# Kernel optimization log

Measured on AMD Instinct MI355X. Metric: run time of the kernel, lower is better.

The kernel has to match this reference:

```python
import jax, jax.numpy as jnp
import numpy as np
import math

D_K = 1024
HEADS = 16
HEAD_DIM = 64

def setup_inputs() -> dict:
    key = jax.random.key(0)
    ks = jax.random.split(key, 9)
    B, S, E = 2, 2048, D_K
    sc = 0.02
    return {
        "x": jax.random.normal(ks[0], (B, S, E), dtype=jnp.float32),
        "mask": 1,
        "Wq": jax.random.normal(ks[1], (E, E), dtype=jnp.float32) * sc,
        "bq": jnp.zeros((E,), dtype=jnp.float32),
        "Wk": jax.random.normal(ks[2], (E, E), dtype=jnp.float32) * sc,
        "bk": jnp.zeros((E,), dtype=jnp.float32),
        "Wv": jax.random.normal(ks[3], (E, E), dtype=jnp.float32) * sc,
        "bv": jnp.zeros((E,), dtype=jnp.float32),
        "Wo": jax.random.normal(ks[4], (E, E), dtype=jnp.float32) * sc,
        "bo": jnp.zeros((E,), dtype=jnp.float32),
    }

def reference(x, mask, Wq, bq, Wk, bk, Wv, bv, Wo, bo):
    B, S, E = x.shape
    H, Dh = HEADS, HEAD_DIM
    # QKV projections; split heads: [B, H, S, Dh]
    q = (x @ Wq + bq).reshape(B, S, H, Dh).transpose(0, 2, 1, 3)
    k = (x @ Wk + bk).reshape(B, S, H, Dh).transpose(0, 2, 1, 3)
    v = (x @ Wv + bv).reshape(B, S, H, Dh).transpose(0, 2, 1, 3)
    # NOTE: original scales by sqrt(d_k) (full model dim), not sqrt(head_dim)
    scores = jnp.einsum('bhsd,bhtd->bhst', q, k) / math.sqrt(E)
    if mask:
        causal = jnp.tril(jnp.ones((S, S), dtype=bool))
        scores = jnp.where(causal[None, None], scores, jnp.float32(-1e9))
    attn = jax.nn.softmax(scores, axis=-1)
    out = jnp.einsum('bhst,bhtd->bhsd', attn, v)  # [B,H,S,Dh]
    out = out.transpose(0, 2, 1, 3).reshape(B, S, E)
    return out @ Wo + bo
```

## Files before the change

### kernel.cpp

```cpp
#include <hip/hip_runtime.h>

#define HEADS  16
#define DH     64
#define SEQ    2048
#define NBATCH 2
#define EMB    1024
#define MTOT   (NBATCH * SEQ)

#define QSCALE 0.045084220027780106f

typedef short  s16x8 __attribute__((ext_vector_type(8)));
typedef float  f32x4 __attribute__((ext_vector_type(4)));
typedef unsigned short u16;
typedef unsigned short u16x4 __attribute__((ext_vector_type(4)));

__device__ __forceinline__ u16 f2bf(float f) {
  unsigned u = __builtin_bit_cast(unsigned, f);
  u += 0x7fffu + ((u >> 16) & 1u);
  return (u16)(u >> 16);
}

__device__ __forceinline__ void gll16(const u16* g, u16* l) {
  __builtin_amdgcn_global_load_lds(
      (const __attribute__((address_space(1))) unsigned int*)g,
      (__attribute__((address_space(3))) unsigned int*)l, 16, 0, 0);
}

__global__ void cvt_x_kernel(const float* __restrict__ x, u16* __restrict__ xb) {
  int i = (blockIdx.x * 256 + threadIdx.x) * 4;
  float4 v = *(const float4*)(x + i);
  u16x4 o;
  o.x = f2bf(v.x); o.y = f2bf(v.y); o.z = f2bf(v.z); o.w = f2bf(v.w);
  *(u16x4*)(xb + i) = o;
}

__global__ void cvt_wt_kernel(const float* __restrict__ Wq, const float* __restrict__ Wk,
                              const float* __restrict__ Wv, const float* __restrict__ Wo,
                              u16* __restrict__ Wqt, u16* __restrict__ Wkt,
                              u16* __restrict__ Wvt, u16* __restrict__ Wot) {
  __shared__ float tile[32][33];
  const float* W; u16* T;
  switch (blockIdx.z) {
    case 0:  W = Wq; T = Wqt; break;
    case 1:  W = Wk; T = Wkt; break;
    case 2:  W = Wv; T = Wvt; break;
    default: W = Wo; T = Wot; break;
  }
  int n0 = blockIdx.x * 32, k0 = blockIdx.y * 32;
  int tx = threadIdx.x, ty = threadIdx.y;
#pragma unroll
  for (int r = 0; r < 32; r += 8)
    tile[ty + r][tx] = W[(size_t)(k0 + ty + r) * EMB + n0 + tx];
  __syncthreads();
#pragma unroll
  for (int r = 0; r < 32; r += 8)
    T[(size_t)(n0 + ty + r) * EMB + k0 + tx] = f2bf(tile[tx][ty + r]);
}

__device__ __forceinline__ void gemm_core(const u16* __restrict__ A, const u16* __restrict__ Bt,
                                          u16* As, u16* Bs, int m0, int n0, f32x4 acc[4][2]) {
  const int tid = threadIdx.x;
  const int lane = tid & 63, w = tid >> 6;
  const int wm = w >> 1, wn = w & 1;
  const int lr = lane & 15, lq = lane >> 4;
#pragma unroll
  for (int i = 0; i < 4; i++)
#pragma unroll
    for (int j = 0; j < 2; j++)
      acc[i][j] = (f32x4){0.f, 0.f, 0.f, 0.f};

  for (int k0 = 0; k0 < EMB; k0 += 64) {
    __syncthreads();
#pragma unroll
    for (int j = 0; j < 4; j++) {
      int c = tid + 256 * j;
      int row = c >> 3, c8 = (c & 7) ^ (row & 7);
      gll16(&A[(size_t)(m0 + row) * EMB + k0 + c8 * 8],
            &As[(w * 64 + 256 * j) * 8]);
    }
#pragma unroll
    for (int j = 0; j < 2; j++) {
      int c = tid + 256 * j;
      int row = c >> 3, c8 = (c & 7) ^ (row & 7);
      gll16(&Bt[(size_t)(n0 + row) * EMB + k0 + c8 * 8],
            &Bs[(w * 64 + 256 * j) * 8]);
    }
    __syncthreads();
#pragma unroll
    for (int kk8 = 0; kk8 < 8; kk8 += 4) {
      s16x8 af[4], bf[2];
#pragma unroll
      for (int i = 0; i < 4; i++) {
        int row = wm * 64 + i * 16 + lr;
        af[i] = *(const s16x8*)&As[row * 64 + (((kk8 + lq) ^ (row & 7)) * 8)];
      }
#pragma unroll
      for (int j = 0; j < 2; j++) {
        int row = wn * 32 + j * 16 + lr;
        bf[j] = *(const s16x8*)&Bs[row * 64 + (((kk8 + lq) ^ (row & 7)) * 8)];
      }
#pragma unroll
      for (int i = 0; i < 4; i++)
#pragma unroll
        for (int j = 0; j < 2; j++)
          acc[i][j] = __builtin_amdgcn_mfma_f32_16x16x32_bf16(af[i], bf[j], acc[i][j], 0, 0, 0);
    }
  }
}

__global__ __launch_bounds__(256) void gemm_qkv(const u16* __restrict__ xb,
                                                const u16* __restrict__ Wqt, const u16* __restrict__ Wkt,
                                                const u16* __restrict__ Wvt,
                                                const float* __restrict__ bq, const float* __restrict__ bk,
                                                const float* __restrict__ bv,
                                                u16* __restrict__ Qb, u16* __restrict__ Kb,
                                                u16* __restrict__ Vtb) {
  __shared__ __align__(16) u16 As[128 * 64];
  __shared__ __align__(16) u16 Bs[64 * 64];
  const int lin  = blockIdx.x + 16 * (blockIdx.y + 32 * blockIdx.z);
  const int job  = (lin & 7) * 192 + (lin >> 3);
  const int mode = job >> 9;
  const int rem  = job & 511;
  const int m0 = (rem >> 4) * 128, n0 = (rem & 15) * 64;

  const u16* Bt; const float* bias; u16* out;
  switch (mode) {
    case 0:  Bt = Wqt; bias = bq; out = Qb;  break;
    case 1:  Bt = Wkt; bias = bk; out = Kb;  break;
    default: Bt = Wvt; bias = bv; out = Vtb; break;
  }
  f32x4 acc[4][2];
  gemm_core(xb, Bt, As, Bs, m0, n0, acc);

  const int tid = threadIdx.x, lane = tid & 63, w = tid >> 6;
  const int wm = w >> 1, wn = w & 1;
  const int lr = lane & 15, lq = lane >> 4;
#pragma unroll
  for (int i = 0; i < 4; i++) {
#pragma unroll
    for (int j = 0; j < 2; j++) {
      int col   = n0 + wn * 32 + j * 16 + lr;
      int mbase = m0 + wm * 64 + i * 16 + lq * 4;
      float bv_ = bias[col];
      int h = col >> 6, d = col & 63;
      if (mode == 0) {
#pragma unroll
        for (int r = 0; r < 4; r++) {
          int m = mbase + r, b = m >> 11, s = m & (SEQ - 1);
          out[((size_t)(b * HEADS + h) * SEQ + s) * DH + d] = f2bf((acc[i][j][r] + bv_) * QSCALE);
        }
      } else if (mode == 1) {
#pragma unroll
        for (int r = 0; r < 4; r++) {
          int m = mbase + r, b = m >> 11, s = m & (SEQ - 1);
          out[((size_t)(b * HEADS + h) * SEQ + s) * DH + d] = f2bf(acc[i][j][r] + bv_);
        }
      } else {
        int b = mbase >> 11, s = mbase & (SEQ - 1);
        u16x4 pk;
        pk.x = f2bf(acc[i][j][0] + bv_);
        pk.y = f2bf(acc[i][j][1] + bv_);
        pk.z = f2bf(acc[i][j][2] + bv_);
        pk.w = f2bf(acc[i][j][3] + bv_);
        *(u16x4*)&out[((size_t)(b * HEADS + h) * DH + d) * SEQ + s] = pk;
      }
    }
  }
}

__global__ __launch_bounds__(256) void gemm_out(const u16* __restrict__ A, const u16* __restrict__ Bt,
                                                const float* __restrict__ bias, float* __restrict__ out) {
  __shared__ __align__(16) u16 As[128 * 64];
  __shared__ __align__(16) u16 Bs[64 * 64];
  const int lin = blockIdx.x + 16 * blockIdx.y;
  const int job = (lin & 7) * 64 + (lin >> 3);
  const int m0 = (job >> 4) * 128, n0 = (job & 15) * 64;
  f32x4 acc[4][2];
  gemm_core(A, Bt, As, Bs, m0, n0, acc);

  const int tid = threadIdx.x, lane = tid & 63, w = tid >> 6;
  const int wm = w >> 1, wn = w & 1;
  const int lr = lane & 15, lq = lane >> 4;
#pragma unroll
  for (int i = 0; i < 4; i++) {
#pragma unroll
    for (int j = 0; j < 2; j++) {
      int col   = n0 + wn * 32 + j * 16 + lr;
      int mbase = m0 + wm * 64 + i * 16 + lq * 4;
      float bv_ = bias[col];
#pragma unroll
      for (int r = 0; r < 4; r++)
        out[(size_t)(mbase + r) * EMB + col] = acc[i][j][r] + bv_;
    }
  }
}

__global__ __launch_bounds__(512, 4) void attn_fwd(const u16* __restrict__ Q,
                                                   const u16* __restrict__ Kg,
                                                   const u16* __restrict__ Vt,
                                                   u16* __restrict__ O) {
  __shared__ __align__(16) u16 smem[33280];
  const int tid = threadIdx.x, lane = tid & 63, w = tid >> 6;
  const int g = w >> 2, wg = w & 3;
  const int lr = lane & 15, lq = lane >> 4;
  const int lin = blockIdx.x + 16 * blockIdx.y;
  const int job = (lin & 7) * 64 + (lin >> 3);
  const int bx = job & 15, bh = job >> 4;
  const int qtA = bx, qtB = 31 - bx;
  const int rowoff = wg * 16;
  u16* Ks = smem + (g ? 11520 : 0);
  u16* Vs = smem + (g ? 16640 : 5120);
  u16* pw = smem + 23040 + w * 1280;
  const size_t qkbase = (size_t)bh * SEQ * DH;
  const size_t vbase  = (size_t)bh * DH * SEQ;
  const u16* kgp = Kg + qkbase;
  const u16* vtp = Vt + vbase;
  const int t256 = tid & 255;
  const int b = bh >> 4, hh = bh & 15;

  {
    int r = t256 >> 4, c = (t256 & 15) * 4;
    u16 one = 0x3F80;
    u16x4 val = (r == 0) ? (u16x4){one, one, one, one} : (u16x4){0, 0, 0, 0};
    *(u16x4*)&Vs[(64 + r) * 80 + c] = val;
  }

  s16x8 qf0, qf1;
  {
    const int myqt0 = g ? qtB : qtA;
    const u16* qp = Q + qkbase + (size_t)(myqt0 * 64 + rowoff + lr) * DH;
    qf0 = *(const s16x8*)&qp[lq * 8];
    qf1 = *(const s16x8*)&qp[32 + lq * 8];
  }
  f32x4 o[4], os;
#pragma unroll
  for (int t = 0; t < 4; t++) o[t] = (f32x4){0.f, 0.f, 0.f, 0.f};
  os = (f32x4){0.f, 0.f, 0.f, 0.f};

  const int srow = t256 >> 3, soff = (t256 & 7) * 8;
  int kt0 = g ? (16 - bx) : 0;
  s16x8 kr0 = *(const s16x8*)&kgp[(size_t)(kt0 * 64 + srow) * DH + soff];
  s16x8 kr1 = *(const s16x8*)&kgp[(size_t)(kt0 * 64 + srow + 32) * DH + soff];
  s16x8 vr0 = *(const s16x8*)&vtp[(size_t)srow * SEQ + kt0 * 64 + soff];
  s16x8 vr1 = *(const s16x8*)&vtp[(size_t)(srow + 32) * SEQ + kt0 * 64 + soff];

  for (int i = 0; i < 17; ++i) {
    __syncthreads();
    *(s16x8*)&Ks[srow * 80 + soff]        = kr0;
    *(s16x8*)&Ks[(srow + 32) * 80 + soff] = kr1;
    *(s16x8*)&Vs[srow * 80 + soff]        = vr0;
    *(s16x8*)&Vs[(srow + 32) * 80 + soff] = vr1;
    __syncthreads();

    {
      bool hn = g ? (i + 1 < 16) : (i + 1 < 17);
      if (hn) {
        int ktn = g ? (17 + i - bx) : ((i + 1 <= qtA) ? (i + 1) : (i - qtA));
        kr0 = *(const s16x8*)&kgp[(size_t)(ktn * 64 + srow) * DH + soff];
        kr1 = *(const s16x8*)&kgp[(size_t)(ktn * 64 + srow + 32) * DH + soff];
        vr0 = *(const s16x8*)&vtp[(size_t)srow * SEQ + ktn * 64 + soff];
        vr1 = *(const s16x8*)&vtp[(size_t)(srow + 32) * SEQ + ktn * 64 + soff];
      }
    }

    if (g == 0 && i == qtA + 1) {
      float inv[4];
#pragma unroll
      for (int r = 0; r < 4; r++) inv[r] = __builtin_amdgcn_rcpf(__shfl(os[r], lq * 16));
#pragma unroll
      for (int t = 0; t < 4; t++)
#pragma unroll
        for (int r = 0; r < 4; r++) {
          int m = b * SEQ + qtA * 64 + rowoff + lq * 4 + r;
          O[(size_t)m * EMB + hh * 64 + t * 16 + lr] = f2bf(o[t][r] * inv[r]);
        }
#pragma unroll
      for (int t = 0; t < 4; t++) o[t] = (f32x4){0.f, 0.f, 0.f, 0.f};
      os = (f32x4){0.f, 0.f, 0.f, 0.f};
      const u16* qp = Q + qkbase + (size_t)(qtB * 64 + rowoff + lr) * DH;
      qf0 = *(const s16x8*)&qp[lq * 8];
      qf1 = *(const s16x8*)&qp[32 + lq * 8];
    }

    const bool docomp = g ? (i < 16) : true;
    if (docomp) {
      f32x4 sc[4];
      __builtin_amdgcn_s_setprio(1);
#pragma unroll
      for (int t = 0; t < 4; t++) {
        s16x8 kf0 = *(const s16x8*)&Ks[(t * 16 + lr) * 80 + lq * 8];
        s16x8 kf1 = *(const s16x8*)&Ks[(t * 16 + lr) * 80 + 32 + lq * 8];
        f32x4 z = (f32x4){0.f, 0.f, 0.f, 0.f};
        z = __builtin_amdgcn_mfma_f32_16x16x32_bf16(qf0, kf0, z, 0, 0, 0);
        z = __builtin_amdgcn_mfma_f32_16x16x32_bf16(qf1, kf1, z, 0, 0, 0);
        sc[t] = z;
      }
      __builtin_amdgcn_s_setprio(0);
      const bool diag = g ? (i == 15) : (i == qtA);
      if (diag) {
#pragma unroll
        for (int t = 0; t < 4; t++)
#pragma unroll
          for (int r = 0; r < 4; r++)
            if ((t * 16 + lr) > (rowoff + lq * 4 + r)) sc[t][r] = -1e9f;
      }
#pragma unroll
      for (int t = 0; t < 4; t++)
#pragma unroll
        for (int r = 0; r < 4; r++)
          sc[t][r] = __builtin_amdgcn_exp2f(sc[t][r]);

#pragma unroll
      for (int t = 0; t < 4; t++)
#pragma unroll
        for (int r = 0; r < 4; r++)
          pw[(lq * 4 + r) * 80 + t * 16 + lr] = f2bf(sc[t][r]);

      __builtin_amdgcn_s_setprio(1);
#pragma unroll
      for (int kc = 0; kc < 2; kc++) {
        s16x8 pf = *(const s16x8*)&pw[lr * 80 + kc * 32 + lq * 8];
#pragma unroll
        for (int t = 0; t < 4; t++) {
          s16x8 vf = *(const s16x8*)&Vs[(t * 16 + lr) * 80 + kc * 32 + lq * 8];
          o[t] = __builtin_amdgcn_mfma_f32_16x16x32_bf16(pf, vf, o[t], 0, 0, 0);
        }
        s16x8 sf = *(const s16x8*)&Vs[(64 + lr) * 80 + kc * 32 + lq * 8];
        os = __builtin_amdgcn_mfma_f32_16x16x32_bf16(pf, sf, os, 0, 0, 0);
      }
      __builtin_amdgcn_s_setprio(0);
    }
  }

  __syncthreads();
  float* Cb = (float*)smem;
  float* Ss = (float*)(smem + 23040);
  if (g == 0) {
#pragma unroll
    for (int t = 0; t < 4; t++)
#pragma unroll
      for (int r = 0; r < 4; r++)
        Cb[(rowoff + lq * 4 + r) * 68 + t * 16 + lr] = o[t][r];
#pragma unroll
    for (int r = 0; r < 4; r++) {
      float s = __shfl(os[r], lq * 16);
      if (lr == 0) Ss[rowoff + lq * 4 + r] = s;
    }
  }
  __syncthreads();
  if (g == 1) {
    float inv[4];
#pragma unroll
    for (int r = 0; r < 4; r++)
      inv[r] = __builtin_amdgcn_rcpf(__shfl(os[r], lq * 16) + Ss[rowoff + lq * 4 + r]);
#pragma unroll
    for (int t = 0; t < 4; t++)
#pragma unroll
      for (int r = 0; r < 4; r++) {
        int m = b * SEQ + qtB * 64 + rowoff + lq * 4 + r;
        float v = o[t][r] + Cb[(rowoff + lq * 4 + r) * 68 + t * 16 + lr];
        O[(size_t)m * EMB + hh * 64 + t * 16 + lr] = f2bf(v * inv[r]);
      }
  }
}

extern "C" void kernel_launch(void* const* d_in, const int* in_sizes, int n_in,
                              void* d_out, int out_size, void* d_ws, size_t ws_size,
                              hipStream_t stream) {
  const float* x  = (const float*)d_in[0];
  const float* Wq = (const float*)d_in[2];
  const float* bq = (const float*)d_in[3];
  const float* Wk = (const float*)d_in[4];
  const float* bk = (const float*)d_in[5];
  const float* Wv = (const float*)d_in[6];
  const float* bv = (const float*)d_in[7];
  const float* Wo = (const float*)d_in[8];
  const float* bo = (const float*)d_in[9];

  char* ws = (char*)d_ws;
  const size_t MB = 1024 * 1024;
  u16* Qb  = (u16*)(ws + 0 * MB);
  u16* Kb  = (u16*)(ws + 8 * MB);
  u16* Vtb = (u16*)(ws + 16 * MB);
  u16* xb  = (u16*)(ws + 24 * MB);
  u16* Ob  = xb;
  u16* Wqt = (u16*)(ws + 32 * MB);
  u16* Wkt = (u16*)(ws + 34 * MB);
  u16* Wvt = (u16*)(ws + 36 * MB);
  u16* Wot = (u16*)(ws + 38 * MB);

  cvt_x_kernel<<<(MTOT * EMB) / (256 * 4), 256, 0, stream>>>(x, xb);
  cvt_wt_kernel<<<dim3(EMB / 32, EMB / 32, 4), dim3(32, 8), 0, stream>>>(
      Wq, Wk, Wv, Wo, Wqt, Wkt, Wvt, Wot);

  gemm_qkv<<<dim3(EMB / 64, MTOT / 128, 3), 256, 0, stream>>>(
      xb, Wqt, Wkt, Wvt, bq, bk, bv, Qb, Kb, Vtb);

  attn_fwd<<<dim3(16, NBATCH * HEADS), 512, 0, stream>>>(Qb, Kb, Vtb, Ob);

  gemm_out<<<dim3(EMB / 64, MTOT / 128), 256, 0, stream>>>(Ob, Wot, bo, (float*)d_out);
}
```

Baseline: 182.5 us.

## Double-buffer GEMM LDS tiles and transpose QK^T MFMA for vectorized P stores

The projection and output GEMMs now use two LDS buffers per operand. The next K-slice is issued with global_load_lds while the current slice is multiplied, and one barrier per iteration replaces two. In attention, the QK^T MFMA operands are swapped so each lane holds four consecutive key columns of one query row. That lets the exp'd probabilities be packed and written to LDS as a single 8-byte store instead of four scalar 2-byte stores, with the causal mask indices adjusted to match. Doubling the GEMM LDS use (48KB per block) may reduce occupancy.

```diff
diff --git a/kernel.cpp b/kernel.cpp
--- a/kernel.cpp
+++ b/kernel.cpp
@@ -57,6 +57,25 @@
     T[(size_t)(n0 + ty + r) * EMB + k0 + tx] = f2bf(tile[tx][ty + r]);
 }
 
+__device__ __forceinline__ void gemm_stage(const u16* __restrict__ A, const u16* __restrict__ Bt,
+                                           u16* As, u16* Bs, int m0, int n0, int k0,
+                                           int tid, int w) {
+#pragma unroll
+  for (int j = 0; j < 4; j++) {
+    int c = tid + 256 * j;
+    int row = c >> 3, c8 = (c & 7) ^ (row & 7);
+    gll16(&A[(size_t)(m0 + row) * EMB + k0 + c8 * 8],
+          &As[(w * 64 + 256 * j) * 8]);
+  }
+#pragma unroll
+  for (int j = 0; j < 2; j++) {
+    int c = tid + 256 * j;
+    int row = c >> 3, c8 = (c & 7) ^ (row & 7);
+    gll16(&Bt[(size_t)(n0 + row) * EMB + k0 + c8 * 8],
+          &Bs[(w * 64 + 256 * j) * 8]);
+  }
+}
+
 __device__ __forceinline__ void gemm_core(const u16* __restrict__ A, const u16* __restrict__ Bt,
                                           u16* As, u16* Bs, int m0, int n0, f32x4 acc[4][2]) {
   const int tid = threadIdx.x;
@@ -69,35 +88,28 @@
     for (int j = 0; j < 2; j++)
       acc[i][j] = (f32x4){0.f, 0.f, 0.f, 0.f};
 
+  gemm_stage(A, Bt, As, Bs, m0, n0, 0, tid, w);
+  __syncthreads();
+
   for (int k0 = 0; k0 < EMB; k0 += 64) {
-    __syncthreads();
-#pragma unroll
-    for (int j = 0; j < 4; j++) {
-      int c = tid + 256 * j;
-      int row = c >> 3, c8 = (c & 7) ^ (row & 7);
-      gll16(&A[(size_t)(m0 + row) * EMB + k0 + c8 * 8],
-            &As[(w * 64 + 256 * j) * 8]);
-    }
-#pragma unroll
-    for (int j = 0; j < 2; j++) {
-      int c = tid + 256 * j;
-      int row = c >> 3, c8 = (c & 7) ^ (row & 7);
-      gll16(&Bt[(size_t)(n0 + row) * EMB + k0 + c8 * 8],
-            &Bs[(w * 64 + 256 * j) * 8]);
-    }
-    __syncthreads();
+    const int cur = (k0 >> 6) & 1;
+    if (k0 + 64 < EMB)
+      gemm_stage(A, Bt, As + (cur ^ 1) * (128 * 64), Bs + (cur ^ 1) * (64 * 64),
+                 m0, n0, k0 + 64, tid, w);
+    const u16* Asc = As + cur * (128 * 64);
+    const u16* Bsc = Bs + cur * (64 * 64);
 #pragma unroll
     for (int kk8 = 0; kk8 < 8; kk8 += 4) {
       s16x8 af[4], bf[2];
 #pragma unroll
       for (int i = 0; i < 4; i++) {
         int row = wm * 64 + i * 16 + lr;
-        af[i] = *(const s16x8*)&As[row * 64 + (((kk8 + lq) ^ (row & 7)) * 8)];
+        af[i] = *(const s16x8*)&Asc[row * 64 + (((kk8 + lq) ^ (row & 7)) * 8)];
       }
 #pragma unroll
       for (int j = 0; j < 2; j++) {
         int row = wn * 32 + j * 16 + lr;
-        bf[j] = *(const s16x8*)&Bs[row * 64 + (((kk8 + lq) ^ (row & 7)) * 8)];
+        bf[j] = *(const s16x8*)&Bsc[row * 64 + (((kk8 + lq) ^ (row & 7)) * 8)];
       }
 #pragma unroll
       for (int i = 0; i < 4; i++)
@@ -105,6 +117,7 @@
         for (int j = 0; j < 2; j++)
           acc[i][j] = __builtin_amdgcn_mfma_f32_16x16x32_bf16(af[i], bf[j], acc[i][j], 0, 0, 0);
     }
+    __syncthreads();
   }
 }
 
@@ -115,8 +128,8 @@
                                                 const float* __restrict__ bv,
                                                 u16* __restrict__ Qb, u16* __restrict__ Kb,
                                                 u16* __restrict__ Vtb) {
-  __shared__ __align__(16) u16 As[128 * 64];
-  __shared__ __align__(16) u16 Bs[64 * 64];
+  __shared__ __align__(16) u16 As[2 * 128 * 64];
+  __shared__ __align__(16) u16 Bs[2 * 64 * 64];
   const int lin  = blockIdx.x + 16 * (blockIdx.y + 32 * blockIdx.z);
   const int job  = (lin & 7) * 192 + (lin >> 3);
   const int mode = job >> 9;
@@ -170,8 +183,8 @@
 
 __global__ __launch_bounds__(256) void gemm_out(const u16* __restrict__ A, const u16* __restrict__ Bt,
                                                 const float* __restrict__ bias, float* __restrict__ out) {
-  __shared__ __align__(16) u16 As[128 * 64];
-  __shared__ __align__(16) u16 Bs[64 * 64];
+  __shared__ __align__(16) u16 As[2 * 128 * 64];
+  __shared__ __align__(16) u16 Bs[2 * 64 * 64];
   const int lin = blockIdx.x + 16 * blockIdx.y;
   const int job = (lin & 7) * 64 + (lin >> 3);
   const int m0 = (job >> 4) * 128, n0 = (job & 15) * 64;
@@ -291,8 +304,8 @@
         s16x8 kf0 = *(const s16x8*)&Ks[(t * 16 + lr) * 80 + lq * 8];
         s16x8 kf1 = *(const s16x8*)&Ks[(t * 16 + lr) * 80 + 32 + lq * 8];
         f32x4 z = (f32x4){0.f, 0.f, 0.f, 0.f};
-        z = __builtin_amdgcn_mfma_f32_16x16x32_bf16(qf0, kf0, z, 0, 0, 0);
-        z = __builtin_amdgcn_mfma_f32_16x16x32_bf16(qf1, kf1, z, 0, 0, 0);
+        z = __builtin_amdgcn_mfma_f32_16x16x32_bf16(kf0, qf0, z, 0, 0, 0);
+        z = __builtin_amdgcn_mfma_f32_16x16x32_bf16(kf1, qf1, z, 0, 0, 0);
         sc[t] = z;
       }
       __builtin_amdgcn_s_setprio(0);
@@ -302,19 +315,17 @@
         for (int t = 0; t < 4; t++)
 #pragma unroll
           for (int r = 0; r < 4; r++)
-            if ((t * 16 + lr) > (rowoff + lq * 4 + r)) sc[t][r] = -1e9f;
-      }
-#pragma unroll
-      for (int t = 0; t < 4; t++)
+            if ((t * 16 + lq * 4 + r) > (rowoff + lr)) sc[t][r] = -1e9f;
+      }
+
+#pragma unroll
+      for (int t = 0; t < 4; t++) {
+        u16x4 pk;
 #pragma unroll
         for (int r = 0; r < 4; r++)
-          sc[t][r] = __builtin_amdgcn_exp2f(sc[t][r]);
-
-#pragma unroll
-      for (int t = 0; t < 4; t++)
-#pragma unroll
-        for (int r = 0; r < 4; r++)
-          pw[(lq * 4 + r) * 80 + t * 16 + lr] = f2bf(sc[t][r]);
+          pk[r] = f2bf(__builtin_amdgcn_exp2f(sc[t][r]));
+        *(u16x4*)&pw[lr * 80 + t * 16 + lq * 4] = pk;
+      }
 
       __builtin_amdgcn_s_setprio(1);
 #pragma unroll
```

After: 188.4 us. 1.03x slower.

## Rewrite QKV GEMM with 256x256 tiles and double-buffered async LDS pipeline

Applied to the files above, without the earlier changes.

Replaces the QKV projection GEMM with a 512-thread kernel using 256x256 output tiles, a two-stage double-buffered global-to-LDS prefetch using explicit vmcnt waits, and MFMA priority hints. It targets the low arithmetic intensity and the unoverlapped load/compute of the old 128x64 tile kernel. The grid shrinks to 192 blocks, which is below the 256 CUs on MI355X, so some CUs sit idle, and the larger tile uses 128KB of LDS and many accumulator registers.

```diff
diff --git a/kernel.cpp b/kernel.cpp
--- a/kernel.cpp
+++ b/kernel.cpp
@@ -57,8 +57,141 @@
     T[(size_t)(n0 + ty + r) * EMB + k0 + tx] = f2bf(tile[tx][ty + r]);
 }
 
-__device__ __forceinline__ void gemm_core(const u16* __restrict__ A, const u16* __restrict__ Bt,
-                                          u16* As, u16* Bs, int m0, int n0, f32x4 acc[4][2]) {
+__global__ __launch_bounds__(512, 2) void gemm_qkv(const u16* __restrict__ xb,
+                                                   const u16* __restrict__ Wqt, const u16* __restrict__ Wkt,
+                                                   const u16* __restrict__ Wvt,
+                                                   const float* __restrict__ bq, const float* __restrict__ bk,
+                                                   const float* __restrict__ bv,
+                                                   u16* __restrict__ Qb, u16* __restrict__ Kb,
+                                                   u16* __restrict__ Vtb) {
+  __shared__ __align__(16) u16 As[2][256 * 64];
+  __shared__ __align__(16) u16 Bs[2][256 * 64];
+  const int tid = threadIdx.x;
+  const int lane = tid & 63, w = tid >> 6;
+  const int wm = w >> 2, wn = w & 3;
+  const int lr = lane & 15, lq = lane >> 4;
+
+  const int lin  = blockIdx.x;
+  const int job  = (lin & 7) * 24 + (lin >> 3);
+  const int mode = job >> 6;
+  const int rem  = job & 63;
+  const int m0 = (rem >> 2) * 256, n0 = (rem & 3) * 256;
+
+  const u16* Bt; const float* bias; u16* out;
+  switch (mode) {
+    case 0:  Bt = Wqt; bias = bq; out = Qb;  break;
+    case 1:  Bt = Wkt; bias = bk; out = Kb;  break;
+    default: Bt = Wvt; bias = bv; out = Vtb; break;
+  }
+
+  f32x4 acc[8][4];
+#pragma unroll
+  for (int i = 0; i < 8; i++)
+#pragma unroll
+    for (int j = 0; j < 4; j++)
+      acc[i][j] = (f32x4){0.f, 0.f, 0.f, 0.f};
+
+  auto stage = [&](int kt, int bi) {
+    const int k0 = kt * 64;
+#pragma unroll
+    for (int j = 0; j < 4; j++) {
+      int c = tid + 512 * j;
+      int row = c >> 3, c8 = (c & 7) ^ (row & 7);
+      gll16(&xb[(size_t)(m0 + row) * EMB + k0 + c8 * 8],
+            &As[bi][(w * 64 + 512 * j) * 8]);
+    }
+#pragma unroll
+    for (int j = 0; j < 4; j++) {
+      int c = tid + 512 * j;
+      int row = c >> 3, c8 = (c & 7) ^ (row & 7);
+      gll16(&Bt[(size_t)(n0 + row) * EMB + k0 + c8 * 8],
+            &Bs[bi][(w * 64 + 512 * j) * 8]);
+    }
+  };
+
+  stage(0, 0);
+  stage(1, 1);
+
+  for (int kt = 0; kt < 16; ++kt) {
+    const int bi = kt & 1;
+    if (kt < 15) asm volatile("s_waitcnt vmcnt(8)" ::: "memory");
+    else         asm volatile("s_waitcnt vmcnt(0)" ::: "memory");
+    __builtin_amdgcn_s_barrier();
+
+    const u16* Asc = As[bi];
+    const u16* Bsc = Bs[bi];
+#pragma unroll
+    for (int kk8 = 0; kk8 < 8; kk8 += 4) {
+      s16x8 bf[4];
+#pragma unroll
+      for (int j = 0; j < 4; j++) {
+        int row = wn * 64 + j * 16 + lr;
+        bf[j] = *(const s16x8*)&Bsc[row * 64 + (((kk8 + lq) ^ (row & 7)) * 8)];
+      }
+#pragma unroll
+      for (int mh = 0; mh < 2; mh++) {
+        s16x8 af[4];
+#pragma unroll
+        for (int i = 0; i < 4; i++) {
+          int row = wm * 128 + mh * 64 + i * 16 + lr;
+          af[i] = *(const s16x8*)&Asc[row * 64 + (((kk8 + lq) ^ (row & 7)) * 8)];
+        }
+        __builtin_amdgcn_s_setprio(1);
+#pragma unroll
+        for (int i = 0; i < 4; i++)
+#pragma unroll
+          for (int j = 0; j < 4; j++)
+            acc[mh * 4 + i][j] =
+                __builtin_amdgcn_mfma_f32_16x16x32_bf16(af[i], bf[j], acc[mh * 4 + i][j], 0, 0, 0);
+        __builtin_amdgcn_s_setprio(0);
+      }
+    }
+
+    asm volatile("s_waitcnt lgkmcnt(0)" ::: "memory");
+    __builtin_amdgcn_s_barrier();
+    __builtin_amdgcn_sched_barrier(0);
+    if (kt + 2 < 16) stage(kt + 2, bi);
+  }
+
+#pragma unroll
+  for (int mh = 0; mh < 2; mh++) {
+#pragma unroll
+    for (int i = 0; i < 4; i++) {
+#pragma unroll
+      for (int j = 0; j < 4; j++) {
+        int col   = n0 + wn * 64 + j * 16 + lr;
+        int mbase = m0 + wm * 128 + mh * 64 + i * 16 + lq * 4;
+        float bv_ = bias[col];
+        int h = col >> 6, d = col & 63;
+        f32x4 a = acc[mh * 4 + i][j];
+        if (mode == 0) {
+#pragma unroll
+          for (int r = 0; r < 4; r++) {
+            int m = mbase + r, b = m >> 11, s = m & (SEQ - 1);
+            out[((size_t)(b * HEADS + h) * SEQ + s) * DH + d] = f2bf((a[r] + bv_) * QSCALE);
+          }
+        } else if (mode == 1) {
+#pragma unroll
+          for (int r = 0; r < 4; r++) {
+            int m = mbase + r, b = m >> 11, s = m & (SEQ - 1);
+            out[((size_t)(b * HEADS + h) * SEQ + s) * DH + d] = f2bf(a[r] + bv_);
+          }
+        } else {
+          int b = mbase >> 11, s = mbase & (SEQ - 1);
+          u16x4 pk;
+          pk.x = f2bf(a[0] + bv_);
+          pk.y = f2bf(a[1] + bv_);
+          pk.z = f2bf(a[2] + bv_);
+          pk.w = f2bf(a[3] + bv_);
+          *(u16x4*)&out[((size_t)(b * HEADS + h) * DH + d) * SEQ + s] = pk;
+        }
+      }
+    }
+  }
+}
+
+__device__ __forceinline__ void gemm_core64(const u16* __restrict__ A, const u16* __restrict__ Bt,
+                                            u16* As, u16* Bs, int m0, int n0, f32x4 acc[4][2]) {
   const int tid = threadIdx.x;
   const int lane = tid & 63, w = tid >> 6;
   const int wm = w >> 1, wn = w & 1;
@@ -104,66 +237,6 @@
 #pragma unroll
         for (int j = 0; j < 2; j++)
           acc[i][j] = __builtin_amdgcn_mfma_f32_16x16x32_bf16(af[i], bf[j], acc[i][j], 0, 0, 0);
-    }
-  }
-}
-
-__global__ __launch_bounds__(256) void gemm_qkv(const u16* __restrict__ xb,
-                                                const u16* __restrict__ Wqt, const u16* __restrict__ Wkt,
-                                                const u16* __restrict__ Wvt,
-                                                const float* __restrict__ bq, const float* __restrict__ bk,
-                                                const float* __restrict__ bv,
-                                                u16* __restrict__ Qb, u16* __restrict__ Kb,
-                                                u16* __restrict__ Vtb) {
-  __shared__ __align__(16) u16 As[128 * 64];
-  __shared__ __align__(16) u16 Bs[64 * 64];
-  const int lin  = blockIdx.x + 16 * (blockIdx.y + 32 * blockIdx.z);
-  const int job  = (lin & 7) * 192 + (lin >> 3);
-  const int mode = job >> 9;
-  const int rem  = job & 511;
-  const int m0 = (rem >> 4) * 128, n0 = (rem & 15) * 64;
-
-  const u16* Bt; const float* bias; u16* out;
-  switch (mode) {
-    case 0:  Bt = Wqt; bias = bq; out = Qb;  break;
-    case 1:  Bt = Wkt; bias = bk; out = Kb;  break;
-    default: Bt = Wvt; bias = bv; out = Vtb; break;
-  }
-  f32x4 acc[4][2];
-  gemm_core(xb, Bt, As, Bs, m0, n0, acc);
-
-  const int tid = threadIdx.x, lane = tid & 63, w = tid >> 6;
-  const int wm = w >> 1, wn = w & 1;
-  const int lr = lane & 15, lq = lane >> 4;
-#pragma unroll
-  for (int i = 0; i < 4; i++) {
-#pragma unroll
-    for (int j = 0; j < 2; j++) {
-      int col   = n0 + wn * 32 + j * 16 + lr;
-      int mbase = m0 + wm * 64 + i * 16 + lq * 4;
-      float bv_ = bias[col];
-      int h = col >> 6, d = col & 63;
-      if (mode == 0) {
-#pragma unroll
-        for (int r = 0; r < 4; r++) {
-          int m = mbase + r, b = m >> 11, s = m & (SEQ - 1);
-          out[((size_t)(b * HEADS + h) * SEQ + s) * DH + d] = f2bf((acc[i][j][r] + bv_) * QSCALE);
-        }
-      } else if (mode == 1) {
-#pragma unroll
-        for (int r = 0; r < 4; r++) {
-          int m = mbase + r, b = m >> 11, s = m & (SEQ - 1);
-          out[((size_t)(b * HEADS + h) * SEQ + s) * DH + d] = f2bf(acc[i][j][r] + bv_);
-        }
-      } else {
-        int b = mbase >> 11, s = mbase & (SEQ - 1);
-        u16x4 pk;
-        pk.x = f2bf(acc[i][j][0] + bv_);
-        pk.y = f2bf(acc[i][j][1] + bv_);
-        pk.z = f2bf(acc[i][j][2] + bv_);
-        pk.w = f2bf(acc[i][j][3] + bv_);
-        *(u16x4*)&out[((size_t)(b * HEADS + h) * DH + d) * SEQ + s] = pk;
-      }
     }
   }
 }
@@ -176,7 +249,7 @@
   const int job = (lin & 7) * 64 + (lin >> 3);
   const int m0 = (job >> 4) * 128, n0 = (job & 15) * 64;
   f32x4 acc[4][2];
-  gemm_core(A, Bt, As, Bs, m0, n0, acc);
+  gemm_core64(A, Bt, As, Bs, m0, n0, acc);
 
   const int tid = threadIdx.x, lane = tid & 63, w = tid >> 6;
   const int wm = w >> 1, wn = w & 1;
@@ -393,7 +466,7 @@
   cvt_wt_kernel<<<dim3(EMB / 32, EMB / 32, 4), dim3(32, 8), 0, stream>>>(
       Wq, Wk, Wv, Wo, Wqt, Wkt, Wvt, Wot);
 
-  gemm_qkv<<<dim3(EMB / 64, MTOT / 128, 3), 256, 0, stream>>>(
+  gemm_qkv<<<dim3(192), 512, 0, stream>>>(
       xb, Wqt, Wkt, Wvt, bq, bk, bv, Qb, Kb, Vtb);
 
   attn_fwd<<<dim3(16, NBATCH * HEADS), 512, 0, stream>>>(Qb, Kb, Vtb, Ob);
```

Result: slower. 186.7 us (+2.3%).
